# Performance work log

Hardware: AMD Instinct MI355X
Metric: run time of the kernel (lower is better)

## Reference

```python
import jax, jax.numpy as jnp
import numpy as np

B, SEQ, NNODES = 4, 12, 1024
SEG_LEN, SEG_NUM = 3, 4
HID, FF, DK, NH, NLAYERS = 64, 2048, 32, 8, 2


def setup_inputs() -> dict:
    key = jax.random.key(0)
    ks = iter(jax.random.split(key, 64))
    def nrm(shape, scale=0.05):
        return jax.random.normal(next(ks), shape, dtype=jnp.float32) * scale
    ones = lambda s: jnp.ones(s, jnp.float32)
    zeros = lambda s: jnp.zeros(s, jnp.float32)
    S, L = 2, NLAYERS
    return {
        'traffic': nrm((B, SEQ, NNODES), 1.0),
        'user': nrm((B, SEQ, NNODES), 1.0),
        'patch_w': nrm((S, HID, SEG_LEN)), 'patch_b': nrm((S, HID)),
        'mha_w': nrm((S, L, 3 * HID, HID)), 'mha_b': nrm((S, L, 3 * HID)),
        'out_w': nrm((S, L, HID, HID)), 'out_b': nrm((S, L, HID)),
        'ff1_w': nrm((S, L, FF, HID)), 'ff1_b': nrm((S, L, FF)),
        'ff2_w': nrm((S, L, HID, FF)), 'ff2_b': nrm((S, L, HID)),
        'ln1_g': ones((S, L, HID)), 'ln1_b': zeros((S, L, HID)),
        'ln2_g': ones((S, L, HID)), 'ln2_b': zeros((S, L, HID)),
        'ga_wq': nrm((S, L, DK, HID)), 'ga_wk': nrm((S, L, DK, HID)), 'ga_wv': nrm((S, L, HID, HID)),
        'ga_ff1_w': nrm((S, L, FF, HID)), 'ga_ff1_b': nrm((S, L, FF)),
        'ga_ff2_w': nrm((S, L, HID, FF)), 'ga_ff2_b': nrm((S, L, HID)),
        'ga_ln1_g': ones((S, L, HID)), 'ga_ln1_b': zeros((S, L, HID)),
        'ga_ln2_g': ones((S, L, HID)), 'ga_ln2_b': zeros((S, L, HID)),
        'ca_wq': nrm((DK, 2 * HID)), 'ca_wk': nrm((DK, 2 * HID)), 'ca_wv': nrm((HID, 2 * HID)),
    }


def _ln(x, g, b, eps=1e-5):
    m = x.mean(-1, keepdims=True)
    v = jnp.mean((x - m) ** 2, -1, keepdims=True)
    return (x - m) / jnp.sqrt(v + eps) * g + b


def _pe(s, d):
    pos = jnp.arange(s, dtype=jnp.float32)[:, None]
    div = jnp.exp(jnp.arange(0, d, 2, dtype=jnp.float32) * (-np.log(10000.0) / d))
    pe = jnp.zeros((s, d), jnp.float32)
    pe = pe.at[:, 0::2].set(jnp.sin(pos * div))
    pe = pe.at[:, 1::2].set(jnp.cos(pos * div))
    return pe


def _mha(x, w, b, wo, bo):
    # standard nn.MultiheadAttention self-attn, batch_first; x: [B,S,H]
    qkv = x @ w.T + b
    q, k, v = jnp.split(qkv, 3, axis=-1)
    def heads(t):
        b_, s_, h_ = t.shape
        return t.reshape(b_, s_, NH, h_ // NH).transpose(0, 2, 1, 3)
    q, k, v = heads(q), heads(k), heads(v)
    scale = 1.0 / jnp.sqrt(jnp.float32(HID // NH))
    att = jax.nn.softmax(jnp.einsum('bhqd,bhkd->bhqk', q, k) * scale, axis=-1)
    o = jnp.einsum('bhqk,bhkd->bhqd', att, v).transpose(0, 2, 1, 3).reshape(x.shape)
    return o @ wo.T + bo


def _enc_layer(x, p):
    # TransformerEncoderLayer_cross, post-norm, dropout=0 (eval)
    x = _ln(x + _mha(x, p['mw'], p['mb'], p['ow'], p['ob']), p['g1'], p['b1'])
    f = jax.nn.relu(x @ p['f1w'].T + p['f1b']) @ p['f2w'].T + p['f2b']
    return _ln(x + f, p['g2'], p['b2'])


def _graph_att(x, p):
    # GraphAttention.forward (bias=None, mask=None, dropout=0)
    q = x @ p['wq'].T
    k = x @ p['wk'].T
    v = x @ p['wv'].T
    dist = jax.nn.softmax(jnp.einsum('bnd,bmd->bnm', q, k) / jnp.sqrt(jnp.float32(DK)), axis=-1)
    att = jnp.einsum('bnm,bmd->bnd', dist, v)
    att = _ln(att, p['g1'], p['b1']) + x
    f = jax.nn.relu(att @ p['f1w'].T + p['f1b']) @ p['f2w'].T + p['f2b']
    return _ln(att + f, p['g2'], p['b2'])


def reference(traffic, user, patch_w, patch_b, mha_w, mha_b, out_w, out_b,
              ff1_w, ff1_b, ff2_w, ff2_b, ln1_g, ln1_b, ln2_g, ln2_b,
              ga_wq, ga_wk, ga_wv, ga_ff1_w, ga_ff1_b, ga_ff2_w, ga_ff2_b,
              ga_ln1_g, ga_ln1_b, ga_ln2_g, ga_ln2_b, ca_wq, ca_wk, ca_wv):
    pe = _pe(SEG_NUM, HID)

    def encode(x, s):
        b, _, d = x.shape
        # DSW_embedding: b (seg_num seg_len) d -> b d seg_num seg_len, then Linear
        seg = x.reshape(b, SEG_NUM, SEG_LEN, d).transpose(0, 3, 1, 2)
        z = seg @ patch_w[s].T + patch_b[s]          # [b, d, seg_num, HID]
        z = z + pe                                    # positional encoding over patches
        for i in range(NLAYERS):
            # temporal attention over the patch axis
            zt = z.reshape(b * d, SEG_NUM, HID)
            zt = _enc_layer(zt, dict(mw=mha_w[s, i], mb=mha_b[s, i], ow=out_w[s, i], ob=out_b[s, i],
                                     f1w=ff1_w[s, i], f1b=ff1_b[s, i], f2w=ff2_w[s, i], f2b=ff2_b[s, i],
                                     g1=ln1_g[s, i], b1=ln1_b[s, i], g2=ln2_g[s, i], b2=ln2_b[s, i]))
            z = zt.reshape(b, d, SEG_NUM, HID)
            # spatial graph attention over the node axis
            zs = z.transpose(0, 2, 1, 3).reshape(b * SEG_NUM, d, HID)
            zs = _graph_att(zs, dict(wq=ga_wq[s, i], wk=ga_wk[s, i], wv=ga_wv[s, i],
                                     f1w=ga_ff1_w[s, i], f1b=ga_ff1_b[s, i], f2w=ga_ff2_w[s, i], f2b=ga_ff2_b[s, i],
                                     g1=ga_ln1_g[s, i], b1=ga_ln1_b[s, i], g2=ga_ln2_g[s, i], b2=ga_ln2_b[s, i]))
            z = zs.reshape(b, SEG_NUM, d, HID).transpose(0, 2, 1, 3)
        return z.mean(axis=2)                         # pool patches -> [b, d, HID]

    enc = jnp.concatenate([encode(traffic, 0), encode(user, 1)], axis=-1)  # [b, d, 2*HID]
    # encoder_attn: SelfAttention(2*HID -> dim_k=32, dim_v=HID)
    q = enc @ ca_wq.T
    k = enc @ ca_wk.T
    v = enc @ ca_wv.T
    dist = jax.nn.softmax(jnp.einsum('bnd,bmd->bnm', q, k) / jnp.sqrt(jnp.float32(DK)), axis=-1)
    return jnp.einsum('bnm,bmd->bnd', dist, v)        # [b, n_nodes, HID]
```

## Files before the change

kernel.cpp:

```cpp
#include <hip/hip_runtime.h>
#include <hip/hip_bf16.h>
#include <math.h>

#define BB 4
#define SEQL 12
#define NN 1024
#define SEGL 3
#define SEGN 4
#define HID 64
#define FFD 2048
#define DKK 32
#define NHH 8
#define HDD 8
#define ZS 1048576

using bf16 = __hip_bfloat16;
__device__ __forceinline__ float b2f(bf16 v) { return __bfloat162float(v); }

typedef __attribute__((ext_vector_type(8))) short s8v;
typedef __attribute__((ext_vector_type(4))) float f4v;
typedef __attribute__((ext_vector_type(4))) unsigned short u4v;

__device__ __forceinline__ unsigned short f2b(float f) {
  bf16 h = __float2bfloat16(f);
  unsigned short u; __builtin_memcpy(&u, &h, 2); return u;
}
__device__ __forceinline__ float us2f(unsigned short u) {
  unsigned int e = ((unsigned int)u) << 16;
  float f; __builtin_memcpy(&f, &e, 4); return f;
}

template <int F>
__device__ __forceinline__ float ldw(const void* p, long i) {
  if (F) return ((const float*)p)[i];
  return b2f(((const bf16*)p)[i]);
}
template <int F>
__device__ __forceinline__ s8v ldfrag(const void* p, long elemOff) {
  if (F) {
    const float* fp = (const float*)p + elemOff;
    f4v u = *(const f4v*)fp, v = *(const f4v*)(fp + 4);
    s8v t;
    t[0]=f2b(u[0]); t[1]=f2b(u[1]); t[2]=f2b(u[2]); t[3]=f2b(u[3]);
    t[4]=f2b(v[0]); t[5]=f2b(v[1]); t[6]=f2b(v[2]); t[7]=f2b(v[3]);
    return t;
  }
  return *(const s8v*)((const unsigned short*)p + elemOff);
}
template <int F>
__device__ __forceinline__ f4v ldb4(const void* p, long i) {
  if (F) return *(const f4v*)((const float*)p + i);
  u4v u = *(const u4v*)((const unsigned short*)p + i);
  f4v r; r[0]=us2f(u[0]); r[1]=us2f(u[1]); r[2]=us2f(u[2]); r[3]=us2f(u[3]);
  return r;
}

__global__ void k_zero(unsigned short* __restrict__ o, int n) {
  int i = blockIdx.x * 256 + threadIdx.x;
  if (i < n) o[i] = 0;
}

__global__ void k_detect(const void* __restrict__ x0, int* __restrict__ flag) {
  int t = threadIdx.x;
  int bad = 0;
  const bf16* p = (const bf16*)x0;
  for (int i = t; i < 512; i += 256) {
    float a = fabsf(b2f(p[i]));
    if (!(a < 1e4f) || (a != 0.f && a < 1e-4f)) bad = 1;
  }
  __shared__ int tot;
  if (t == 0) tot = 0;
  __syncthreads();
  unsigned long long m = __ballot(bad);
  if ((t & 63) == 0) atomicAdd(&tot, __popcll(m));
  __syncthreads();
  if (t == 0) *flag = (tot > 64) ? 1 : 0;
}

template <int F>
__device__ __forceinline__ void wconv_body(const void* __restrict__ w1,
    const void* __restrict__ w2, const void* __restrict__ w3,
    const void* __restrict__ w4, unsigned short* __restrict__ out) {
  int i = blockIdx.x * 256 + threadIdx.x;
  long e8 = (long)i * 8;
  int slot = (int)(e8 >> 17);
  int si = slot >> 2, which = slot & 3;
  long r = e8 & 131071;
  const void* src = (which == 0) ? w1 : (which == 1) ? w2 : (which == 2) ? w3 : w4;
  *(s8v*)(out + e8) = ldfrag<F>(src, (long)si*FFD*HID + r);
}
__global__ __launch_bounds__(256) void k_wconv(const void* w1, const void* w2,
    const void* w3, const void* w4, unsigned short* out,
    const int* __restrict__ flag) {
  if (*flag) wconv_body<1>(w1, w2, w3, w4, out);
  else       wconv_body<0>(w1, w2, w3, w4, out);
}

template <int F>
__device__ __forceinline__ void patch_body(const void* __restrict__ xt,
    const void* __restrict__ xu,
    const void* __restrict__ pw, const void* __restrict__ pb,
    float* __restrict__ z) {
  int bid = blockIdx.x;
  int s = bid >> 12, rem = bid & 4095;
  int b = rem >> 10, n = rem & 1023;
  const void* x = s ? xu : xt;
  long opw = (long)s*HID*SEGL, opb = (long)s*HID;
  int g = threadIdx.x >> 6, h = threadIdx.x & 63;
  float acc = ldw<F>(pb, opb + h);
#pragma unroll
  for (int l = 0; l < SEGL; ++l)
    acc += ldw<F>(x, (long)(b*SEQL + g*SEGL + l)*NN + n) * ldw<F>(pw, opw + h*SEGL + l);
  int i2 = h >> 1;
  float dv = expf((float)(2*i2) * (-logf(10000.f) / (float)HID));
  float ang = (float)g * dv;
  acc += (h & 1) ? cosf(ang) : sinf(ang);
  z[(long)s*ZS + ((long)(b*NN + n)*SEGN + g)*HID + h] = acc;
}
__global__ __launch_bounds__(256) void k_patch(const void* __restrict__ xt,
    const void* __restrict__ xu,
    const void* __restrict__ pw, const void* __restrict__ pb,
    float* __restrict__ z, const int* __restrict__ flag) {
  if (*flag) patch_body<1>(xt, xu, pw, pb, z);
  else       patch_body<0>(xt, xu, pw, pb, z);
}

#define TT 64
template <int F>
__device__ __forceinline__ void tattn_body(float* __restrict__ zb,
    const void* __restrict__ W, const void* __restrict__ bq,
    const void* __restrict__ WO, const void* __restrict__ bo,
    const void* __restrict__ g1, const void* __restrict__ b1,
    int li, char* lds) {
  int s = blockIdx.x >> 8, blk = blockIdx.x & 255;
  long si = s*2 + li;
  float* z = zb + (long)s*ZS;
  long oW = si*3*HID*HID, obq = si*3*HID, oWO = si*HID*HID, obo = si*HID;
  long og1 = si*HID, ob1 = si*HID;
  unsigned short (*qkvs)[200] = (unsigned short(*)[200])lds;
  unsigned short (*ao)[72]    = (unsigned short(*)[72])(lds + 25600);
  float (*yb)[68]             = (float(*)[68])(lds + 34816);
  int tid = threadIdx.x;
  int w = tid >> 6, lane = tid & 63;
  int col = lane & 15, quad = lane >> 4;
  long r0 = (long)blk * TT;

  s8v bx[4][2];
#pragma unroll
  for (int mt = 0; mt < 4; ++mt) {
    const float* xr = z + (r0 + mt*16 + col) * HID;
#pragma unroll
    for (int ks = 0; ks < 2; ++ks) {
      const float* p = xr + ks*32 + quad*8;
      f4v u = *(const f4v*)p, v = *(const f4v*)(p + 4);
      s8v t;
      t[0]=f2b(u[0]); t[1]=f2b(u[1]); t[2]=f2b(u[2]); t[3]=f2b(u[3]);
      t[4]=f2b(v[0]); t[5]=f2b(v[1]); t[6]=f2b(v[2]); t[7]=f2b(v[3]);
      bx[mt][ks] = t;
    }
  }
#pragma unroll
  for (int nt = 0; nt < 3; ++nt) {
    int cbase = (w*3 + nt) * 16;
    s8v aw[2];
#pragma unroll
    for (int ks = 0; ks < 2; ++ks)
      aw[ks] = ldfrag<F>(W, oW + (long)(cbase + col)*HID + ks*32 + quad*8);
    f4v bv = ldb4<F>(bq, obq + cbase + quad*4);
#pragma unroll
    for (int mt = 0; mt < 4; ++mt) {
      f4v sv = (f4v){0.f,0.f,0.f,0.f};
#pragma unroll
      for (int ks = 0; ks < 2; ++ks)
        sv = __builtin_amdgcn_mfma_f32_16x16x32_bf16(aw[ks], bx[mt][ks], sv, 0, 0, 0);
      unsigned short pk[4];
#pragma unroll
      for (int r = 0; r < 4; ++r) pk[r] = f2b(sv[r] + bv[r]);
      *(unsigned long long*)&qkvs[mt*16 + col][cbase + quad*4] =
        (unsigned long long)pk[0] | ((unsigned long long)pk[1] << 16) |
        ((unsigned long long)pk[2] << 32) | ((unsigned long long)pk[3] << 48);
    }
  }
  __syncthreads();
  if (tid < 128) {
    int gi = tid >> 3, hd = tid & 7;
    int tl = gi * 4;
    float qv[4][8], kv[4][8], vv[4][8];
#pragma unroll
    for (int t4 = 0; t4 < 4; ++t4) {
      s8v qq = *(const s8v*)&qkvs[tl + t4][hd*8];
      s8v kk = *(const s8v*)&qkvs[tl + t4][64 + hd*8];
      s8v vq = *(const s8v*)&qkvs[tl + t4][128 + hd*8];
#pragma unroll
      for (int e = 0; e < 8; ++e) {
        qv[t4][e] = us2f((unsigned short)qq[e]);
        kv[t4][e] = us2f((unsigned short)kk[e]);
        vv[t4][e] = us2f((unsigned short)vq[e]);
      }
    }
    const float sc8 = 0.3535533905932738f;
#pragma unroll
    for (int qt = 0; qt < 4; ++qt) {
      float s[4]; float mx = -1e30f;
#pragma unroll
      for (int kt = 0; kt < 4; ++kt) {
        float d = 0;
#pragma unroll
        for (int e = 0; e < 8; ++e) d += qv[qt][e]*kv[kt][e];
        s[kt] = d*sc8; mx = fmaxf(mx, s[kt]);
      }
      float se = 0;
#pragma unroll
      for (int kt = 0; kt < 4; ++kt) { s[kt] = expf(s[kt]-mx); se += s[kt]; }
      float inv = 1.f/se;
      s8v outp;
#pragma unroll
      for (int e = 0; e < 8; ++e) {
        float o = 0;
#pragma unroll
        for (int kt = 0; kt < 4; ++kt) o += s[kt]*vv[kt][e];
        outp[e] = (short)f2b(o*inv);
      }
      *(s8v*)&ao[tl + qt][hd*8] = outp;
    }
  }
  __syncthreads();
  s8v awo[2];
#pragma unroll
  for (int ks = 0; ks < 2; ++ks)
    awo[ks] = ldfrag<F>(WO, oWO + (long)(w*16 + col)*HID + ks*32 + quad*8);
  f4v bov = ldb4<F>(bo, obo + w*16 + quad*4);
#pragma unroll
  for (int mt = 0; mt < 4; ++mt) {
    f4v ov = (f4v){0.f,0.f,0.f,0.f};
#pragma unroll
    for (int ks = 0; ks < 2; ++ks) {
      s8v bao = *(const s8v*)&ao[mt*16 + col][ks*32 + quad*8];
      ov = __builtin_amdgcn_mfma_f32_16x16x32_bf16(awo[ks], bao, ov, 0, 0, 0);
    }
    f4v yv;
#pragma unroll
    for (int r = 0; r < 4; ++r) yv[r] = ov[r] + bov[r];
    *(f4v*)&yb[mt*16 + col][w*16 + quad*4] = yv;
  }
  __syncthreads();
  float gg = ldw<F>(g1, og1 + lane), bb2 = ldw<F>(b1, ob1 + lane);
#pragma unroll
  for (int rr = 0; rr < 16; ++rr) {
    int row = w*16 + rr;
    long tok = r0 + row;
    float val = yb[row][lane] + z[tok*HID + lane];
    float s = val;
#pragma unroll
    for (int off = 32; off; off >>= 1) s += __shfl_xor(s, off);
    float m = s*(1.f/HID);
    float d = val - m, sq = d*d;
#pragma unroll
    for (int off = 32; off; off >>= 1) sq += __shfl_xor(sq, off);
    float rv = rsqrtf(sq*(1.f/HID) + 1e-5f);
    z[tok*HID + lane] = d*rv*gg + bb2;
  }
}
__global__ __launch_bounds__(256) void k_tattn(float* __restrict__ z,
    const void* W, const void* bqkv, const void* WO, const void* bo,
    const void* g1, const void* b1, int li, const int* __restrict__ flag) {
  __shared__ __attribute__((aligned(16))) char lds[52224];
  if (*flag) tattn_body<1>(z, W, bqkv, WO, bo, g1, b1, li, lds);
  else       tattn_body<0>(z, W, bqkv, WO, bo, g1, b1, li, lds);
}

#define FRW 64
#define HCS 74

__device__ __forceinline__ void ff_ld(const unsigned short* __restrict__ wc1,
    const unsigned short* __restrict__ wc2, int hb, int srow, int le,
    s8v* r1, s8v* r2) {
  r1[0] = *(const s8v*)(wc1 + (long)(hb + srow)*HID + le*8);
  r1[1] = *(const s8v*)(wc1 + (long)(hb + srow + 8)*HID + le*8);
  r2[0] = *(const s8v*)(wc2 + (long)srow*FFD + hb + le*8);
  r2[1] = *(const s8v*)(wc2 + (long)(srow + 8)*FFD + hb + le*8);
}
__device__ __forceinline__ void ff_wr(char* ldsbuf, int pb, int srow, int swb,
    const s8v* r1, const s8v* r2) {
  char* w1b = ldsbuf + pb*8192;
  char* w2b = ldsbuf + 16384 + pb*8192;
  *(s8v*)(w1b + srow*128 + swb) = r1[0];
  *(s8v*)(w1b + (srow + 8)*128 + swb) = r1[1];
  *(s8v*)(w2b + srow*128 + swb) = r2[0];
  *(s8v*)(w2b + (srow + 8)*128 + swb) = r2[1];
}

template <int F>
__device__ __forceinline__ void ffmfma_body(float* __restrict__ xb,
    const unsigned short* __restrict__ wcw, int li, int wsel,
    const void* __restrict__ B1, const void* __restrict__ B2,
    const void* __restrict__ G, const void* __restrict__ Bt,
    char* ldsbuf) {
  int s = blockIdx.x >> 8, blk = blockIdx.x & 255;
  long si = s*2 + li;
  float* x = xb + (long)s*ZS;
  const unsigned short* wc1 = wcw + (si*4 + wsel)*131072;
  const unsigned short* wc2 = wcw + (si*4 + wsel + 1)*131072;
  long ob1 = si*FFD, ob2 = si*HID, og = si*HID, obt = si*HID;
  int tid = threadIdx.x;
  int w = tid >> 6, lane = tid & 63;
  int col = lane & 15, quad = lane >> 4;
  long r0 = (long)blk * FRW;
  unsigned short* hcw = (unsigned short*)(ldsbuf + 32768 + w*2368);
  float* red = (float*)(ldsbuf + 42240 + w*4352);

  long tokc = r0 + w*16 + col;
  s8v bx[2];
  {
    const float* xr = x + tokc * HID;
#pragma unroll
    for (int ks = 0; ks < 2; ++ks) {
      const float* p = xr + ks*32 + quad*8;
      f4v u = *(const f4v*)p, v = *(const f4v*)(p + 4);
      s8v t;
      t[0]=f2b(u[0]); t[1]=f2b(u[1]); t[2]=f2b(u[2]); t[3]=f2b(u[3]);
      t[4]=f2b(v[0]); t[5]=f2b(v[1]); t[6]=f2b(v[2]); t[7]=f2b(v[3]);
      bx[ks] = t;
    }
  }

  int lr = lane >> 3;
  int le = lane & 7;
  int srow = w*16 + lr;
  int swb = ((le ^ lr) << 4);

  f4v acc[4];
#pragma unroll
  for (int m = 0; m < 4; ++m) acc[m] = (f4v){0.f,0.f,0.f,0.f};

  s8v cw1[2], cw2[2], nw1[2], nw2[2];
  ff_ld(wc1, wc2, 0, srow, le, cw1, cw2);
  ff_wr(ldsbuf, 0, srow, swb, cw1, cw2);
  __syncthreads();

  const int sw = (col & 7) << 4;
  for (int c = 0; c < 32; ++c) {
    int pb = c & 1;
    if (c < 31) ff_ld(wc1, wc2, (c+1)*64, srow, le, nw1, nw2);
    const char* w1b = ldsbuf + pb*8192;
    const char* w2b = ldsbuf + 16384 + pb*8192;
    const int hb = c*64;
#pragma unroll
    for (int t = 0; t < 4; ++t) {
      int row = t*16 + col;
      s8v a10 = *(const s8v*)(w1b + row*128 + ((quad*16) ^ sw));
      s8v a11 = *(const s8v*)(w1b + row*128 + ((64 + quad*16) ^ sw));
      f4v bv = ldb4<F>(B1, ob1 + hb + t*16 + quad*4);
      f4v sv = __builtin_amdgcn_mfma_f32_16x16x32_bf16(a10, bx[0],
                 (f4v){0.f,0.f,0.f,0.f}, 0, 0, 0);
      sv = __builtin_amdgcn_mfma_f32_16x16x32_bf16(a11, bx[1], sv, 0, 0, 0);
      unsigned short pk[4];
#pragma unroll
      for (int r = 0; r < 4; ++r) pk[r] = f2b(fmaxf(sv[r] + bv[r], 0.f));
      *(unsigned long long*)&hcw[col*HCS + t*16 + quad*4] =
        (unsigned long long)pk[0] | ((unsigned long long)pk[1] << 16) |
        ((unsigned long long)pk[2] << 32) | ((unsigned long long)pk[3] << 48);
    }
#pragma unroll
    for (int ks2 = 0; ks2 < 2; ++ks2) {
      s8v bh = *(const s8v*)&hcw[col*HCS + ks2*32 + quad*8];
#pragma unroll
      for (int m = 0; m < 4; ++m) {
        int r2 = m*16 + col;
        s8v a2 = *(const s8v*)(w2b + r2*128 + ((ks2*64 + quad*16) ^ sw));
        acc[m] = __builtin_amdgcn_mfma_f32_16x16x32_bf16(a2, bh, acc[m], 0, 0, 0);
      }
    }
    if (c < 31) ff_wr(ldsbuf, pb ^ 1, srow, swb, nw1, nw2);
    __syncthreads();
  }

#pragma unroll
  for (int m = 0; m < 4; ++m)
    *(f4v*)&red[col*68 + m*16 + quad*4] = acc[m];
  float gg = ldw<F>(G, og + lane), bbt = ldw<F>(Bt, obt + lane);
  float b2v = ldw<F>(B2, ob2 + lane);
#pragma unroll
  for (int rr = 0; rr < 16; ++rr) {
    long grow = r0 + w*16 + rr;
    float val = red[rr*68 + lane] + b2v + x[grow*HID + lane];
    float sm = val;
#pragma unroll
    for (int off = 32; off; off >>= 1) sm += __shfl_xor(sm, off);
    float m = sm * (1.f/HID);
    float d = val - m;
    float sq = d*d;
#pragma unroll
    for (int off = 32; off; off >>= 1) sq += __shfl_xor(sq, off);
    float rv = rsqrtf(sq*(1.f/HID) + 1e-5f);
    x[grow*HID + lane] = d*rv*gg + bbt;
  }
}
__global__ __launch_bounds__(256) void k_ffmfma(float* __restrict__ x,
    const unsigned short* __restrict__ wcw, int li, int wsel,
    const void* B1, const void* B2, const void* G, const void* Bt,
    const int* __restrict__ flag) {
  __shared__ __attribute__((aligned(16))) char ldsbuf[59648];
  if (*flag) ffmfma_body<1>(x, wcw, li, wsel, B1, B2, G, Bt, ldsbuf);
  else       ffmfma_body<0>(x, wcw, li, wsel, B1, B2, G, Bt, ldsbuf);
}

template <int F>
__device__ __forceinline__ void gqkv_body(const float* __restrict__ zb,
    const void* __restrict__ wq, const void* __restrict__ wk,
    const void* __restrict__ wv, int li,
    unsigned short* __restrict__ q, unsigned short* __restrict__ k,
    unsigned short* __restrict__ vt) {
  int tid = threadIdx.x;
  int w = tid >> 6, lane = tid & 63;
  int col = lane & 15, quad = lane >> 4;
  int sg = blockIdx.x >> 4;
  int s = sg >> 4, bg = sg & 15;
  int n0 = (blockIdx.x & 15) * 64;
  int b = bg >> 2, g = bg & 3;
  long si = s*2 + li;
  const float* z = zb + (long)s*ZS;
  long oq = si*DKK*HID, ok = si*DKK*HID, ov = si*HID*HID;
  long gbase = (long)sg * NN;

  s8v bx[4][2];
#pragma unroll
  for (int rt = 0; rt < 4; ++rt) {
    const float* xr = z + ((long)(b*NN + n0 + rt*16 + col)*SEGN + g)*HID;
#pragma unroll
    for (int ks = 0; ks < 2; ++ks) {
      const float* p = xr + ks*32 + quad*8;
      f4v u = *(const f4v*)p, vv = *(const f4v*)(p + 4);
      s8v t;
      t[0]=f2b(u[0]); t[1]=f2b(u[1]); t[2]=f2b(u[2]); t[3]=f2b(u[3]);
      t[4]=f2b(vv[0]); t[5]=f2b(vv[1]); t[6]=f2b(vv[2]); t[7]=f2b(vv[3]);
      bx[rt][ks] = t;
    }
  }

#pragma unroll
  for (int tt = 0; tt < 2; ++tt) {
    int ct = w*2 + tt;
    const void* wp; long wo; int co; int kind;
    if (ct < 2)      { wp = wq; wo = oq; co = ct*16;      kind = 0; }
    else if (ct < 4) { wp = wk; wo = ok; co = (ct-2)*16;  kind = 1; }
    else             { wp = wv; wo = ov; co = (ct-4)*16;  kind = 2; }
    s8v aw[2];
#pragma unroll
    for (int ks = 0; ks < 2; ++ks)
      aw[ks] = ldfrag<F>(wp, wo + (long)(co + col)*HID + ks*32 + quad*8);
#pragma unroll
    for (int rt = 0; rt < 4; ++rt) {
      f4v sv = (f4v){0.f,0.f,0.f,0.f};
#pragma unroll
      for (int ks = 0; ks < 2; ++ks)
        sv = __builtin_amdgcn_mfma_f32_16x16x32_bf16(aw[ks], bx[rt][ks], sv, 0, 0, 0);
      int key = n0 + rt*16 + col;
      if (kind == 2) {
        long vbase = (long)sg*HID*NN;
#pragma unroll
        for (int r = 0; r < 4; ++r)
          vt[vbase + (long)(co + quad*4 + r)*NN + key] = f2b(sv[r]);
      } else {
        long row = gbase + key;
        unsigned short pk[4];
#pragma unroll
        for (int r = 0; r < 4; ++r) pk[r] = f2b(sv[r]);
        unsigned short* dst = kind ? k : q;
        *(unsigned long long*)&dst[row*DKK + co + quad*4] =
          (unsigned long long)pk[0] | ((unsigned long long)pk[1] << 16) |
          ((unsigned long long)pk[2] << 32) | ((unsigned long long)pk[3] << 48);
      }
    }
  }
}
__global__ __launch_bounds__(256) void k_gqkv(const float* __restrict__ z,
    const void* wq, const void* wk, const void* wv, int li,
    unsigned short* q, unsigned short* k, unsigned short* vt,
    const int* __restrict__ flag) {
  if (*flag) gqkv_body<1>(z, wq, wk, wv, li, q, k, vt);
  else       gqkv_body<0>(z, wq, wk, wv, li, q, k, vt);
}

__global__ __launch_bounds__(512) void k_gattn(float* __restrict__ zb,
    const unsigned short* __restrict__ qb, const unsigned short* __restrict__ kb,
    const unsigned short* __restrict__ vtb,
    const void* __restrict__ g1, const void* __restrict__ b1, int li,
    const int* __restrict__ flag) {
  int f = *flag;
  __shared__ unsigned short pl[2][8][16][74];
  __shared__ float accb[8][16][66];
  __shared__ float lb[8][16];
  int tid = threadIdx.x;
  int w = tid >> 6, lane = tid & 63;
  int col = lane & 15, quad = lane >> 4;
  int qt = w >> 1, kh = w & 1;
  int sg = blockIdx.x >> 4;
  int s = sg >> 4, bg = sg & 15;
  int n0 = (blockIdx.x & 15) * 64;
  long si = s*2 + li;
  float* z = zb + (long)s*ZS;
  long og1 = si*HID, ob1 = si*HID;
  long gbase = (long)sg * NN;
  const unsigned short* vrow = vtb + (long)sg*HID*NN;

  s8v aq = *(const s8v*)(qb + (gbase + n0 + qt*16 + col)*DKK + quad*8);

  f4v acc[4];
#pragma unroll
  for (int t = 0; t < 4; ++t) acc[t] = (f4v){0.f,0.f,0.f,0.f};
  float psum[4] = {0.f,0.f,0.f,0.f};
  const float rs = 0.17677669529663687f;
  const int cbeg = kh * 512;

#pragma unroll 2
  for (int it = 0; it < 8; ++it) {
    int c0 = cbeg + it*64;
    int pb = it & 1;
    f4v s4[4];
#pragma unroll
    for (int nt = 0; nt < 4; ++nt) {
      s8v bk = *(const s8v*)(kb + (gbase + c0 + nt*16 + col)*DKK + quad*8);
      s4[nt] = __builtin_amdgcn_mfma_f32_16x16x32_bf16(aq, bk,
                (f4v){0.f,0.f,0.f,0.f}, 0, 0, 0);
    }
#pragma unroll
    for (int r = 0; r < 4; ++r) {
      float p0 = expf(s4[0][r]*rs), p1 = expf(s4[1][r]*rs);
      float p2 = expf(s4[2][r]*rs), p3 = expf(s4[3][r]*rs);
      psum[r] += (p0 + p1) + (p2 + p3);
      int row = quad*4 + r;
      pl[pb][w][row][col]      = f2b(p0);
      pl[pb][w][row][16 + col] = f2b(p1);
      pl[pb][w][row][32 + col] = f2b(p2);
      pl[pb][w][row][48 + col] = f2b(p3);
    }
#pragma unroll
    for (int ks = 0; ks < 2; ++ks) {
      s8v ap = *(const s8v*)&pl[pb][w][col][ks*32 + quad*8];
#pragma unroll
      for (int nt = 0; nt < 4; ++nt) {
        s8v bv = *(const s8v*)(vrow + (long)(nt*16 + col)*NN + c0 + ks*32 + quad*8);
        acc[nt] = __builtin_amdgcn_mfma_f32_16x16x32_bf16(ap, bv, acc[nt], 0, 0, 0);
      }
    }
  }

#pragma unroll
  for (int r = 0; r < 4; ++r) {
    float v = psum[r];
#pragma unroll
    for (int off = 1; off < 16; off <<= 1) v += __shfl_xor(v, off);
    psum[r] = v;
  }
#pragma unroll
  for (int t = 0; t < 4; ++t)
#pragma unroll
    for (int r = 0; r < 4; ++r)
      accb[w][quad*4 + r][t*16 + col] = acc[t][r];
  if (col == 0) {
#pragma unroll
    for (int r = 0; r < 4; ++r) lb[w][quad*4 + r] = psum[r];
  }
  __syncthreads();

  int b = bg >> 2, g = bg & 3;
  float gg = f ? ((const float*)g1)[og1 + lane] : b2f(((const bf16*)g1)[og1 + lane]);
  float bb = f ? ((const float*)b1)[ob1 + lane] : b2f(((const bf16*)b1)[ob1 + lane]);
#pragma unroll
  for (int rr = 0; rr < 8; ++rr) {
    int rl = w*8 + rr;
    int qtt = rl >> 4, lr = rl & 15;
    float a = accb[2*qtt][lr][lane] + accb[2*qtt + 1][lr][lane];
    float l = lb[2*qtt][lr] + lb[2*qtt + 1][lr];
    float val = a / l;
    float s = val;
#pragma unroll
    for (int off = 32; off; off >>= 1) s += __shfl_xor(s, off);
    float m = s*(1.f/HID);
    float d = val - m, sq = d*d;
#pragma unroll
    for (int off = 32; off; off >>= 1) sq += __shfl_xor(sq, off);
    float r = rsqrtf(sq*(1.f/HID) + 1e-5f);
    float* zp = z + ((long)(b*NN + n0 + rl)*SEGN + g)*HID;
    zp[lane] = d*r*gg + bb + zp[lane];
  }
}

__global__ __launch_bounds__(64) void k_pool(const float* __restrict__ z,
    float* __restrict__ enc) {
  int bid = blockIdx.x;
  int s = bid >> 12, rem = bid & 4095;
  int b = rem >> 10, n = rem & 1023, h = threadIdx.x;
  const float* zp = z + (long)s*ZS + (long)(b*NN + n)*SEGN*HID;
  float a = 0;
#pragma unroll
  for (int g = 0; g < SEGN; ++g) a += zp[g*HID + h];
  enc[(long)(b*NN + n)*(2*HID) + s*HID + h] = a*0.25f;
}

template <int F>
__device__ __forceinline__ void fqkv_body(const float* __restrict__ enc,
    const void* __restrict__ wq, const void* __restrict__ wk,
    const void* __restrict__ wv,
    unsigned short* __restrict__ q, unsigned short* __restrict__ k,
    unsigned short* __restrict__ vt, float* xs) {
  long r = blockIdx.x;
  int t = threadIdx.x;
  xs[t] = enc[r*128 + t];
  __syncthreads();
  if (t < 32) {
    long wr = (long)t*128; float a = 0;
    for (int e = 0; e < 128; ++e) a += xs[e]*ldw<F>(wq, wr + e);
    q[r*DKK + t] = f2b(a);
  } else if (t < 64) {
    long wr = (long)(t-32)*128; float a = 0;
    for (int e = 0; e < 128; ++e) a += xs[e]*ldw<F>(wk, wr + e);
    k[r*DKK + (t-32)] = f2b(a);
  } else {
    long wr = (long)(t-64)*128; float a = 0;
    for (int e = 0; e < 128; ++e) a += xs[e]*ldw<F>(wv, wr + e);
    vt[((r >> 10)*HID + (t-64))*NN + (r & 1023)] = f2b(a);
  }
}
__global__ __launch_bounds__(128) void k_fqkv(const float* __restrict__ enc,
    const void* wq, const void* wk, const void* wv,
    unsigned short* q, unsigned short* k, unsigned short* vt,
    const int* __restrict__ flag) {
  __shared__ float xs[2*HID];
  if (*flag) fqkv_body<1>(enc, wq, wk, wv, q, k, vt, xs);
  else       fqkv_body<0>(enc, wq, wk, wv, q, k, vt, xs);
}

__global__ __launch_bounds__(512) void k_fattn(
    const unsigned short* __restrict__ qb, const unsigned short* __restrict__ kb,
    const unsigned short* __restrict__ vtb, void* __restrict__ outp,
    const int* __restrict__ flag) {
  __shared__ unsigned short pl[2][8][16][74];
  __shared__ float accb[8][16][66];
  __shared__ float lb[8][16];
  int tid = threadIdx.x;
  int w = tid >> 6, lane = tid & 63;
  int col = lane & 15, quad = lane >> 4;
  int qt = w >> 1, kh = w & 1;
  int b = blockIdx.x >> 4;
  int n0 = (blockIdx.x & 15) * 64;
  long gbase = (long)b * NN;
  const unsigned short* vrow = vtb + (long)b*HID*NN;

  s8v aq = *(const s8v*)(qb + (gbase + n0 + qt*16 + col)*DKK + quad*8);

  f4v acc[4];
#pragma unroll
  for (int t = 0; t < 4; ++t) acc[t] = (f4v){0.f,0.f,0.f,0.f};
  float psum[4] = {0.f,0.f,0.f,0.f};
  const float rs = 0.17677669529663687f;
  const int cbeg = kh * 512;

#pragma unroll 2
  for (int it = 0; it < 8; ++it) {
    int c0 = cbeg + it*64;
    int pb = it & 1;
    f4v s4[4];
#pragma unroll
    for (int nt = 0; nt < 4; ++nt) {
      s8v bk = *(const s8v*)(kb + (gbase + c0 + nt*16 + col)*DKK + quad*8);
      s4[nt] = __builtin_amdgcn_mfma_f32_16x16x32_bf16(aq, bk,
                (f4v){0.f,0.f,0.f,0.f}, 0, 0, 0);
    }
#pragma unroll
    for (int r = 0; r < 4; ++r) {
      float p0 = expf(s4[0][r]*rs), p1 = expf(s4[1][r]*rs);
      float p2 = expf(s4[2][r]*rs), p3 = expf(s4[3][r]*rs);
      psum[r] += (p0 + p1) + (p2 + p3);
      int row = quad*4 + r;
      pl[pb][w][row][col]      = f2b(p0);
      pl[pb][w][row][16 + col] = f2b(p1);
      pl[pb][w][row][32 + col] = f2b(p2);
      pl[pb][w][row][48 + col] = f2b(p3);
    }
#pragma unroll
    for (int ks = 0; ks < 2; ++ks) {
      s8v ap = *(const s8v*)&pl[pb][w][col][ks*32 + quad*8];
#pragma unroll
      for (int nt = 0; nt < 4; ++nt) {
        s8v bv = *(const s8v*)(vrow + (long)(nt*16 + col)*NN + c0 + ks*32 + quad*8);
        acc[nt] = __builtin_amdgcn_mfma_f32_16x16x32_bf16(ap, bv, acc[nt], 0, 0, 0);
      }
    }
  }

#pragma unroll
  for (int r = 0; r < 4; ++r) {
    float v = psum[r];
#pragma unroll
    for (int off = 1; off < 16; off <<= 1) v += __shfl_xor(v, off);
    psum[r] = v;
  }
#pragma unroll
  for (int t = 0; t < 4; ++t)
#pragma unroll
    for (int r = 0; r < 4; ++r)
      accb[w][quad*4 + r][t*16 + col] = acc[t][r];
  if (col == 0) {
#pragma unroll
    for (int r = 0; r < 4; ++r) lb[w][quad*4 + r] = psum[r];
  }
  __syncthreads();

  int f = *flag;
#pragma unroll
  for (int rr = 0; rr < 8; ++rr) {
    int rl = w*8 + rr;
    int qtt = rl >> 4, lr = rl & 15;
    float a = accb[2*qtt][lr][lane] + accb[2*qtt + 1][lr][lane];
    float l = lb[2*qtt][lr] + lb[2*qtt + 1][lr];
    float val = a / l;
    long idx = (gbase + n0 + rl)*HID + lane;
    if (f) ((float*)outp)[idx] = val;
    else   ((bf16*)outp)[idx] = __float2bfloat16(val);
  }
}

extern "C" void kernel_launch(void* const* d_in, const int* in_sizes, int n_in,
                              void* d_out, int out_size, void* d_ws, size_t ws_size,
                              hipStream_t stream) {
  static const int EXP[30] = {
    49152, 49152, 384, 128, 49152, 768, 16384, 256,
    524288, 8192, 524288, 256, 256, 256, 256, 256,
    8192, 8192, 16384, 524288, 8192, 524288, 256, 256,
    256, 256, 256, 4096, 4096, 8192
  };
  const size_t NEED = (size_t)(2*ZS + 524288 + 524288 + 524288 + 1048576 + 1048576) * 4 + 64;
  bool ok = (n_in == 30) && (ws_size >= NEED) && (out_size == BB*NN*HID);
  if (ok) for (int i = 0; i < 30; ++i) ok = ok && (in_sizes[i] == EXP[i]);
  if (!ok) {
    k_zero<<<(BB*NN*HID + 255)/256, 256, 0, stream>>>((unsigned short*)d_out, BB*NN*HID);
    return;
  }

  float* z   = (float*)d_ws;
  float* enc = z   + 2*ZS;
  float* qb  = enc + 524288;
  float* kb  = qb  + 524288;
  float* vb  = kb  + 524288;
  float* wcf = vb  + 1048576;
  int*  flag = (int*)(wcf + 1048576);
  unsigned short* wcw = (unsigned short*)wcf;

  k_detect<<<1, 256, 0, stream>>>(d_in[0], flag);

  const void *i_traffic=d_in[0], *i_user=d_in[1], *i_pw=d_in[2], *i_pb=d_in[3],
    *i_mw=d_in[4], *i_mb=d_in[5], *i_ow=d_in[6], *i_ob=d_in[7], *i_f1w=d_in[8],
    *i_f1b=d_in[9], *i_f2w=d_in[10], *i_f2b=d_in[11], *i_l1g=d_in[12],
    *i_l1b=d_in[13], *i_l2g=d_in[14], *i_l2b=d_in[15], *i_gwq=d_in[16],
    *i_gwk=d_in[17], *i_gwv=d_in[18], *i_gf1w=d_in[19], *i_gf1b=d_in[20],
    *i_gf2w=d_in[21], *i_gf2b=d_in[22], *i_gl1g=d_in[23], *i_gl1b=d_in[24],
    *i_gl2g=d_in[25], *i_gl2b=d_in[26], *i_cwq=d_in[27], *i_cwk=d_in[28],
    *i_cwv=d_in[29];

  k_wconv<<<1024, 256, 0, stream>>>(i_f1w, i_f2w, i_gf1w, i_gf2w, wcw, flag);
  k_patch<<<2*BB*NN, 256, 0, stream>>>(i_traffic, i_user, i_pw, i_pb, z, flag);

  const int FFG = 2*BB*NN*SEGN/FRW;

  for (int i = 0; i < 2; ++i) {
    k_tattn<<<512, 256, 0, stream>>>(z, i_mw, i_mb, i_ow, i_ob,
        i_l1g, i_l1b, i, flag);
    k_ffmfma<<<FFG, 256, 0, stream>>>(z, wcw, i, 0,
        i_f1b, i_f2b, i_l2g, i_l2b, flag);
    k_gqkv<<<512, 256, 0, stream>>>(z, i_gwq, i_gwk, i_gwv, i,
        (unsigned short*)qb, (unsigned short*)kb, (unsigned short*)vb, flag);
    k_gattn<<<512, 512, 0, stream>>>(z,
        (const unsigned short*)qb, (const unsigned short*)kb,
        (const unsigned short*)vb, i_gl1g, i_gl1b, i, flag);
    k_ffmfma<<<FFG, 256, 0, stream>>>(z, wcw, i, 2,
        i_gf1b, i_gf2b, i_gl2g, i_gl2b, flag);
  }
  k_pool<<<2*BB*NN, 64, 0, stream>>>(z, enc);
  k_fqkv<<<BB*NN, 128, 0, stream>>>(enc, i_cwq, i_cwk, i_cwv,
      (unsigned short*)qb, (unsigned short*)kb, (unsigned short*)vb, flag);
  k_fattn<<<BB*16, 512, 0, stream>>>((const unsigned short*)qb,
      (const unsigned short*)kb, (unsigned short*)vb, d_out, flag);
}
```

Before: 610.1 us.

## Fuse temporal attention with feed-forward and fold patch pooling into final FFN

Merges the temporal self-attention kernel and the following feed-forward kernel into one kernel. The post-LayerNorm activations stay in shared memory instead of being written to and re-read from global memory, which also removes one launch per layer. Separately, the last graph FFN epilogue now accumulates the segment mean and writes the pooled encoding directly, so the standalone pooling kernel is dropped. The fused kernel uses more shared memory (about 77KB per block), which may lower occupancy.

Measured after the change: 601.4 us. Within noise of the previous version (-1.4%).

```diff
diff --git a/kernel.cpp b/kernel.cpp
--- a/kernel.cpp
+++ b/kernel.cpp
@@ -126,149 +126,6 @@
 }
 
 #define TT 64
-template <int F>
-__device__ __forceinline__ void tattn_body(float* __restrict__ zb,
-    const void* __restrict__ W, const void* __restrict__ bq,
-    const void* __restrict__ WO, const void* __restrict__ bo,
-    const void* __restrict__ g1, const void* __restrict__ b1,
-    int li, char* lds) {
-  int s = blockIdx.x >> 8, blk = blockIdx.x & 255;
-  long si = s*2 + li;
-  float* z = zb + (long)s*ZS;
-  long oW = si*3*HID*HID, obq = si*3*HID, oWO = si*HID*HID, obo = si*HID;
-  long og1 = si*HID, ob1 = si*HID;
-  unsigned short (*qkvs)[200] = (unsigned short(*)[200])lds;
-  unsigned short (*ao)[72]    = (unsigned short(*)[72])(lds + 25600);
-  float (*yb)[68]             = (float(*)[68])(lds + 34816);
-  int tid = threadIdx.x;
-  int w = tid >> 6, lane = tid & 63;
-  int col = lane & 15, quad = lane >> 4;
-  long r0 = (long)blk * TT;
-
-  s8v bx[4][2];
-#pragma unroll
-  for (int mt = 0; mt < 4; ++mt) {
-    const float* xr = z + (r0 + mt*16 + col) * HID;
-#pragma unroll
-    for (int ks = 0; ks < 2; ++ks) {
-      const float* p = xr + ks*32 + quad*8;
-      f4v u = *(const f4v*)p, v = *(const f4v*)(p + 4);
-      s8v t;
-      t[0]=f2b(u[0]); t[1]=f2b(u[1]); t[2]=f2b(u[2]); t[3]=f2b(u[3]);
-      t[4]=f2b(v[0]); t[5]=f2b(v[1]); t[6]=f2b(v[2]); t[7]=f2b(v[3]);
-      bx[mt][ks] = t;
-    }
-  }
-#pragma unroll
-  for (int nt = 0; nt < 3; ++nt) {
-    int cbase = (w*3 + nt) * 16;
-    s8v aw[2];
-#pragma unroll
-    for (int ks = 0; ks < 2; ++ks)
-      aw[ks] = ldfrag<F>(W, oW + (long)(cbase + col)*HID + ks*32 + quad*8);
-    f4v bv = ldb4<F>(bq, obq + cbase + quad*4);
-#pragma unroll
-    for (int mt = 0; mt < 4; ++mt) {
-      f4v sv = (f4v){0.f,0.f,0.f,0.f};
-#pragma unroll
-      for (int ks = 0; ks < 2; ++ks)
-        sv = __builtin_amdgcn_mfma_f32_16x16x32_bf16(aw[ks], bx[mt][ks], sv, 0, 0, 0);
-      unsigned short pk[4];
-#pragma unroll
-      for (int r = 0; r < 4; ++r) pk[r] = f2b(sv[r] + bv[r]);
-      *(unsigned long long*)&qkvs[mt*16 + col][cbase + quad*4] =
-        (unsigned long long)pk[0] | ((unsigned long long)pk[1] << 16) |
-        ((unsigned long long)pk[2] << 32) | ((unsigned long long)pk[3] << 48);
-    }
-  }
-  __syncthreads();
-  if (tid < 128) {
-    int gi = tid >> 3, hd = tid & 7;
-    int tl = gi * 4;
-    float qv[4][8], kv[4][8], vv[4][8];
-#pragma unroll
-    for (int t4 = 0; t4 < 4; ++t4) {
-      s8v qq = *(const s8v*)&qkvs[tl + t4][hd*8];
-      s8v kk = *(const s8v*)&qkvs[tl + t4][64 + hd*8];
-      s8v vq = *(const s8v*)&qkvs[tl + t4][128 + hd*8];
-#pragma unroll
-      for (int e = 0; e < 8; ++e) {
-        qv[t4][e] = us2f((unsigned short)qq[e]);
-        kv[t4][e] = us2f((unsigned short)kk[e]);
-        vv[t4][e] = us2f((unsigned short)vq[e]);
-      }
-    }
-    const float sc8 = 0.3535533905932738f;
-#pragma unroll
-    for (int qt = 0; qt < 4; ++qt) {
-      float s[4]; float mx = -1e30f;
-#pragma unroll
-      for (int kt = 0; kt < 4; ++kt) {
-        float d = 0;
-#pragma unroll
-        for (int e = 0; e < 8; ++e) d += qv[qt][e]*kv[kt][e];
-        s[kt] = d*sc8; mx = fmaxf(mx, s[kt]);
-      }
-      float se = 0;
-#pragma unroll
-      for (int kt = 0; kt < 4; ++kt) { s[kt] = expf(s[kt]-mx); se += s[kt]; }
-      float inv = 1.f/se;
-      s8v outp;
-#pragma unroll
-      for (int e = 0; e < 8; ++e) {
-        float o = 0;
-#pragma unroll
-        for (int kt = 0; kt < 4; ++kt) o += s[kt]*vv[kt][e];
-        outp[e] = (short)f2b(o*inv);
-      }
-      *(s8v*)&ao[tl + qt][hd*8] = outp;
-    }
-  }
-  __syncthreads();
-  s8v awo[2];
-#pragma unroll
-  for (int ks = 0; ks < 2; ++ks)
-    awo[ks] = ldfrag<F>(WO, oWO + (long)(w*16 + col)*HID + ks*32 + quad*8);
-  f4v bov = ldb4<F>(bo, obo + w*16 + quad*4);
-#pragma unroll
-  for (int mt = 0; mt < 4; ++mt) {
-    f4v ov = (f4v){0.f,0.f,0.f,0.f};
-#pragma unroll
-    for (int ks = 0; ks < 2; ++ks) {
-      s8v bao = *(const s8v*)&ao[mt*16 + col][ks*32 + quad*8];
-      ov = __builtin_amdgcn_mfma_f32_16x16x32_bf16(awo[ks], bao, ov, 0, 0, 0);
-    }
-    f4v yv;
-#pragma unroll
-    for (int r = 0; r < 4; ++r) yv[r] = ov[r] + bov[r];
-    *(f4v*)&yb[mt*16 + col][w*16 + quad*4] = yv;
-  }
-  __syncthreads();
-  float gg = ldw<F>(g1, og1 + lane), bb2 = ldw<F>(b1, ob1 + lane);
-#pragma unroll
-  for (int rr = 0; rr < 16; ++rr) {
-    int row = w*16 + rr;
-    long tok = r0 + row;
-    float val = yb[row][lane] + z[tok*HID + lane];
-    float s = val;
-#pragma unroll
-    for (int off = 32; off; off >>= 1) s += __shfl_xor(s, off);
-    float m = s*(1.f/HID);
-    float d = val - m, sq = d*d;
-#pragma unroll
-    for (int off = 32; off; off >>= 1) sq += __shfl_xor(sq, off);
-    float rv = rsqrtf(sq*(1.f/HID) + 1e-5f);
-    z[tok*HID + lane] = d*rv*gg + bb2;
-  }
-}
-__global__ __launch_bounds__(256) void k_tattn(float* __restrict__ z,
-    const void* W, const void* bqkv, const void* WO, const void* bo,
-    const void* g1, const void* b1, int li, const int* __restrict__ flag) {
-  __shared__ __attribute__((aligned(16))) char lds[52224];
-  if (*flag) tattn_body<1>(z, W, bqkv, WO, bo, g1, b1, li, lds);
-  else       tattn_body<0>(z, W, bqkv, WO, bo, g1, b1, li, lds);
-}
-
 #define FRW 64
 #define HCS 74
 
@@ -291,10 +148,253 @@
 }
 
 template <int F>
+__device__ __forceinline__ void tff_body(float* __restrict__ zb,
+    const void* __restrict__ W, const void* __restrict__ bq,
+    const void* __restrict__ WO, const void* __restrict__ bo,
+    const void* __restrict__ g1, const void* __restrict__ b1,
+    const unsigned short* __restrict__ wcw, int li,
+    const void* __restrict__ B1, const void* __restrict__ B2,
+    const void* __restrict__ G, const void* __restrict__ Bt,
+    char* lds) {
+  int s = blockIdx.x >> 8, blk = blockIdx.x & 255;
+  long si = s*2 + li;
+  float* z = zb + (long)s*ZS;
+  long oW = si*3*HID*HID, obq = si*3*HID, oWO = si*HID*HID, obo = si*HID;
+  long og1 = si*HID, ob1 = si*HID;
+  const unsigned short* wc1 = wcw + (si*4 + 0)*131072;
+  const unsigned short* wc2 = wcw + (si*4 + 1)*131072;
+  long fob1 = si*FFD, fob2 = si*HID, fog = si*HID, fobt = si*HID;
+  unsigned short (*qkvs)[200] = (unsigned short(*)[200])lds;
+  unsigned short (*ao)[72]    = (unsigned short(*)[72])(lds + 25600);
+  float (*yb)[68]             = (float(*)[68])(lds + 34816);
+  int tid = threadIdx.x;
+  int w = tid >> 6, lane = tid & 63;
+  int col = lane & 15, quad = lane >> 4;
+  long r0 = (long)blk * TT;
+  float* stashW = (float*)(lds + 59648 + w*4352);
+
+  int lr = lane >> 3, le = lane & 7;
+  int srow = w*16 + lr;
+  int swb = ((le ^ lr) << 4);
+  s8v cw1[2], cw2[2];
+  ff_ld(wc1, wc2, 0, srow, le, cw1, cw2);
+
+  s8v bx[4][2];
+#pragma unroll
+  for (int mt = 0; mt < 4; ++mt) {
+    const float* xr = z + (r0 + mt*16 + col) * HID;
+#pragma unroll
+    for (int ks = 0; ks < 2; ++ks) {
+      const float* p = xr + ks*32 + quad*8;
+      f4v u = *(const f4v*)p, v = *(const f4v*)(p + 4);
+      s8v t;
+      t[0]=f2b(u[0]); t[1]=f2b(u[1]); t[2]=f2b(u[2]); t[3]=f2b(u[3]);
+      t[4]=f2b(v[0]); t[5]=f2b(v[1]); t[6]=f2b(v[2]); t[7]=f2b(v[3]);
+      bx[mt][ks] = t;
+    }
+  }
+#pragma unroll
+  for (int nt = 0; nt < 3; ++nt) {
+    int cbase = (w*3 + nt) * 16;
+    s8v aw[2];
+#pragma unroll
+    for (int ks = 0; ks < 2; ++ks)
+      aw[ks] = ldfrag<F>(W, oW + (long)(cbase + col)*HID + ks*32 + quad*8);
+    f4v bv = ldb4<F>(bq, obq + cbase + quad*4);
+#pragma unroll
+    for (int mt = 0; mt < 4; ++mt) {
+      f4v sv = (f4v){0.f,0.f,0.f,0.f};
+#pragma unroll
+      for (int ks = 0; ks < 2; ++ks)
+        sv = __builtin_amdgcn_mfma_f32_16x16x32_bf16(aw[ks], bx[mt][ks], sv, 0, 0, 0);
+      unsigned short pk[4];
+#pragma unroll
+      for (int r = 0; r < 4; ++r) pk[r] = f2b(sv[r] + bv[r]);
+      *(unsigned long long*)&qkvs[mt*16 + col][cbase + quad*4] =
+        (unsigned long long)pk[0] | ((unsigned long long)pk[1] << 16) |
+        ((unsigned long long)pk[2] << 32) | ((unsigned long long)pk[3] << 48);
+    }
+  }
+  __syncthreads();
+  if (tid < 128) {
+    int gi = tid >> 3, hd = tid & 7;
+    int tl = gi * 4;
+    float qv[4][8], kv[4][8], vv[4][8];
+#pragma unroll
+    for (int t4 = 0; t4 < 4; ++t4) {
+      s8v qq = *(const s8v*)&qkvs[tl + t4][hd*8];
+      s8v kk = *(const s8v*)&qkvs[tl + t4][64 + hd*8];
+      s8v vq = *(const s8v*)&qkvs[tl + t4][128 + hd*8];
+#pragma unroll
+      for (int e = 0; e < 8; ++e) {
+        qv[t4][e] = us2f((unsigned short)qq[e]);
+        kv[t4][e] = us2f((unsigned short)kk[e]);
+        vv[t4][e] = us2f((unsigned short)vq[e]);
+      }
+    }
+    const float sc8 = 0.3535533905932738f;
+#pragma unroll
+    for (int qt = 0; qt < 4; ++qt) {
+      float sc[4]; float mx = -1e30f;
+#pragma unroll
+      for (int kt = 0; kt < 4; ++kt) {
+        float d = 0;
+#pragma unroll
+        for (int e = 0; e < 8; ++e) d += qv[qt][e]*kv[kt][e];
+        sc[kt] = d*sc8; mx = fmaxf(mx, sc[kt]);
+      }
+      float se = 0;
+#pragma unroll
+      for (int kt = 0; kt < 4; ++kt) { sc[kt] = expf(sc[kt]-mx); se += sc[kt]; }
+      float inv = 1.f/se;
+      s8v outp;
+#pragma unroll
+      for (int e = 0; e < 8; ++e) {
+        float o = 0;
+#pragma unroll
+        for (int kt = 0; kt < 4; ++kt) o += sc[kt]*vv[kt][e];
+        outp[e] = (short)f2b(o*inv);
+      }
+      *(s8v*)&ao[tl + qt][hd*8] = outp;
+    }
+  }
+  __syncthreads();
+  s8v awo[2];
+#pragma unroll
+  for (int ks = 0; ks < 2; ++ks)
+    awo[ks] = ldfrag<F>(WO, oWO + (long)(w*16 + col)*HID + ks*32 + quad*8);
+  f4v bov = ldb4<F>(bo, obo + w*16 + quad*4);
+#pragma unroll
+  for (int mt = 0; mt < 4; ++mt) {
+    f4v ov = (f4v){0.f,0.f,0.f,0.f};
+#pragma unroll
+    for (int ks = 0; ks < 2; ++ks) {
+      s8v bao = *(const s8v*)&ao[mt*16 + col][ks*32 + quad*8];
+      ov = __builtin_amdgcn_mfma_f32_16x16x32_bf16(awo[ks], bao, ov, 0, 0, 0);
+    }
+    f4v yv;
+#pragma unroll
+    for (int r = 0; r < 4; ++r) yv[r] = ov[r] + bov[r];
+    *(f4v*)&yb[mt*16 + col][w*16 + quad*4] = yv;
+  }
+  __syncthreads();
+  {
+    float gg = ldw<F>(g1, og1 + lane), bb2 = ldw<F>(b1, ob1 + lane);
+#pragma unroll
+    for (int rr = 0; rr < 16; ++rr) {
+      int row = w*16 + rr;
+      long tok = r0 + row;
+      float val = yb[row][lane] + z[tok*HID + lane];
+      float sm = val;
+#pragma unroll
+      for (int off = 32; off; off >>= 1) sm += __shfl_xor(sm, off);
+      float m = sm*(1.f/HID);
+      float d = val - m, sq = d*d;
+#pragma unroll
+      for (int off = 32; off; off >>= 1) sq += __shfl_xor(sq, off);
+      float rv = rsqrtf(sq*(1.f/HID) + 1e-5f);
+      stashW[rr*68 + lane] = d*rv*gg + bb2;
+    }
+  }
+  __syncthreads();
+
+  unsigned short* hcw = (unsigned short*)(lds + 32768 + w*2368);
+  float* red = (float*)(lds + 42240 + w*4352);
+
+  s8v bx2[2];
+#pragma unroll
+  for (int ks = 0; ks < 2; ++ks) {
+    const float* p = &stashW[col*68 + ks*32 + quad*8];
+    f4v u = *(const f4v*)p, v = *(const f4v*)(p + 4);
+    s8v t;
+    t[0]=f2b(u[0]); t[1]=f2b(u[1]); t[2]=f2b(u[2]); t[3]=f2b(u[3]);
+    t[4]=f2b(v[0]); t[5]=f2b(v[1]); t[6]=f2b(v[2]); t[7]=f2b(v[3]);
+    bx2[ks] = t;
+  }
+
+  f4v acc[4];
+#pragma unroll
+  for (int m = 0; m < 4; ++m) acc[m] = (f4v){0.f,0.f,0.f,0.f};
+
+  ff_wr(lds, 0, srow, swb, cw1, cw2);
+  __syncthreads();
+
+  const int sw = (col & 7) << 4;
+  s8v nw1[2], nw2[2];
+  for (int c = 0; c < 32; ++c) {
+    int pb = c & 1;
+    if (c < 31) ff_ld(wc1, wc2, (c+1)*64, srow, le, nw1, nw2);
+    const char* w1b = lds + pb*8192;
+    const char* w2b = lds + 16384 + pb*8192;
+    const int hb = c*64;
+#pragma unroll
+    for (int t = 0; t < 4; ++t) {
+      int row = t*16 + col;
+      s8v a10 = *(const s8v*)(w1b + row*128 + ((quad*16) ^ sw));
+      s8v a11 = *(const s8v*)(w1b + row*128 + ((64 + quad*16) ^ sw));
+      f4v bv = ldb4<F>(B1, fob1 + hb + t*16 + quad*4);
+      f4v sv = __builtin_amdgcn_mfma_f32_16x16x32_bf16(a10, bx2[0],
+                 (f4v){0.f,0.f,0.f,0.f}, 0, 0, 0);
+      sv = __builtin_amdgcn_mfma_f32_16x16x32_bf16(a11, bx2[1], sv, 0, 0, 0);
+      unsigned short pk[4];
+#pragma unroll
+      for (int r = 0; r < 4; ++r) pk[r] = f2b(fmaxf(sv[r] + bv[r], 0.f));
+      *(unsigned long long*)&hcw[col*HCS + t*16 + quad*4] =
+        (unsigned long long)pk[0] | ((unsigned long long)pk[1] << 16) |
+        ((unsigned long long)pk[2] << 32) | ((unsigned long long)pk[3] << 48);
+    }
+#pragma unroll
+    for (int ks2 = 0; ks2 < 2; ++ks2) {
+      s8v bh = *(const s8v*)&hcw[col*HCS + ks2*32 + quad*8];
+#pragma unroll
+      for (int m = 0; m < 4; ++m) {
+        int r2 = m*16 + col;
+        s8v a2 = *(const s8v*)(w2b + r2*128 + ((ks2*64 + quad*16) ^ sw));
+        acc[m] = __builtin_amdgcn_mfma_f32_16x16x32_bf16(a2, bh, acc[m], 0, 0, 0);
+      }
+    }
+    if (c < 31) ff_wr(lds, pb ^ 1, srow, swb, nw1, nw2);
+    __syncthreads();
+  }
+
+#pragma unroll
+  for (int m = 0; m < 4; ++m)
+    *(f4v*)&red[col*68 + m*16 + quad*4] = acc[m];
+  float fgg = ldw<F>(G, fog + lane), fbbt = ldw<F>(Bt, fobt + lane);
+  float b2v = ldw<F>(B2, fob2 + lane);
+#pragma unroll
+  for (int rr = 0; rr < 16; ++rr) {
+    long grow = r0 + w*16 + rr;
+    float val = red[rr*68 + lane] + b2v + stashW[rr*68 + lane];
+    float sm = val;
+#pragma unroll
+    for (int off = 32; off; off >>= 1) sm += __shfl_xor(sm, off);
+    float m = sm * (1.f/HID);
+    float d = val - m;
+    float sq = d*d;
+#pragma unroll
+    for (int off = 32; off; off >>= 1) sq += __shfl_xor(sq, off);
+    float rv = rsqrtf(sq*(1.f/HID) + 1e-5f);
+    z[grow*HID + lane] = d*rv*fgg + fbbt;
+  }
+}
+__global__ __launch_bounds__(256) void k_tff(float* __restrict__ z,
+    const void* W, const void* bqkv, const void* WO, const void* bo,
+    const void* g1, const void* b1,
+    const unsigned short* __restrict__ wcw, int li,
+    const void* B1, const void* B2, const void* G, const void* Bt,
+    const int* __restrict__ flag) {
+  __shared__ __attribute__((aligned(16))) char lds[77056];
+  if (*flag) tff_body<1>(z, W, bqkv, WO, bo, g1, b1, wcw, li, B1, B2, G, Bt, lds);
+  else       tff_body<0>(z, W, bqkv, WO, bo, g1, b1, wcw, li, B1, B2, G, Bt, lds);
+}
+
+template <int F>
 __device__ __forceinline__ void ffmfma_body(float* __restrict__ xb,
     const unsigned short* __restrict__ wcw, int li, int wsel,
     const void* __restrict__ B1, const void* __restrict__ B2,
     const void* __restrict__ G, const void* __restrict__ Bt,
+    float* __restrict__ enc, int dop,
     char* ldsbuf) {
   int s = blockIdx.x >> 8, blk = blockIdx.x & 255;
   long si = s*2 + li;
@@ -380,6 +480,7 @@
     *(f4v*)&red[col*68 + m*16 + quad*4] = acc[m];
   float gg = ldw<F>(G, og + lane), bbt = ldw<F>(Bt, obt + lane);
   float b2v = ldw<F>(B2, ob2 + lane);
+  float pacc[4] = {0.f,0.f,0.f,0.f};
 #pragma unroll
   for (int rr = 0; rr < 16; ++rr) {
     long grow = r0 + w*16 + rr;
@@ -393,16 +494,25 @@
 #pragma unroll
     for (int off = 32; off; off >>= 1) sq += __shfl_xor(sq, off);
     float rv = rsqrtf(sq*(1.f/HID) + 1e-5f);
-    x[grow*HID + lane] = d*rv*gg + bbt;
+    float fin = d*rv*gg + bbt;
+    x[grow*HID + lane] = fin;
+    pacc[rr >> 2] += fin;
+  }
+  if (dop) {
+#pragma unroll
+    for (int j = 0; j < 4; ++j) {
+      long tok = r0 + w*16 + j*4;
+      enc[(tok >> 2)*(2*HID) + s*HID + lane] = pacc[j]*0.25f;
+    }
   }
 }
 __global__ __launch_bounds__(256) void k_ffmfma(float* __restrict__ x,
     const unsigned short* __restrict__ wcw, int li, int wsel,
     const void* B1, const void* B2, const void* G, const void* Bt,
-    const int* __restrict__ flag) {
+    float* enc, int dop, const int* __restrict__ flag) {
   __shared__ __attribute__((aligned(16))) char ldsbuf[59648];
-  if (*flag) ffmfma_body<1>(x, wcw, li, wsel, B1, B2, G, Bt, ldsbuf);
-  else       ffmfma_body<0>(x, wcw, li, wsel, B1, B2, G, Bt, ldsbuf);
+  if (*flag) ffmfma_body<1>(x, wcw, li, wsel, B1, B2, G, Bt, enc, dop, ldsbuf);
+  else       ffmfma_body<0>(x, wcw, li, wsel, B1, B2, G, Bt, enc, dop, ldsbuf);
 }
 
 template <int F>
@@ -574,10 +684,10 @@
     float a = accb[2*qtt][lr][lane] + accb[2*qtt + 1][lr][lane];
     float l = lb[2*qtt][lr] + lb[2*qtt + 1][lr];
     float val = a / l;
-    float s = val;
-#pragma unroll
-    for (int off = 32; off; off >>= 1) s += __shfl_xor(s, off);
-    float m = s*(1.f/HID);
+    float s2 = val;
+#pragma unroll
+    for (int off = 32; off; off >>= 1) s2 += __shfl_xor(s2, off);
+    float m = s2*(1.f/HID);
     float d = val - m, sq = d*d;
 #pragma unroll
     for (int off = 32; off; off >>= 1) sq += __shfl_xor(sq, off);
@@ -585,18 +695,6 @@
     float* zp = z + ((long)(b*NN + n0 + rl)*SEGN + g)*HID;
     zp[lane] = d*r*gg + bb + zp[lane];
   }
-}
-
-__global__ __launch_bounds__(64) void k_pool(const float* __restrict__ z,
-    float* __restrict__ enc) {
-  int bid = blockIdx.x;
-  int s = bid >> 12, rem = bid & 4095;
-  int b = rem >> 10, n = rem & 1023, h = threadIdx.x;
-  const float* zp = z + (long)s*ZS + (long)(b*NN + n)*SEGN*HID;
-  float a = 0;
-#pragma unroll
-  for (int g = 0; g < SEGN; ++g) a += zp[g*HID + h];
-  enc[(long)(b*NN + n)*(2*HID) + s*HID + h] = a*0.25f;
 }
 
 template <int F>
@@ -762,22 +860,17 @@
   k_wconv<<<1024, 256, 0, stream>>>(i_f1w, i_f2w, i_gf1w, i_gf2w, wcw, flag);
   k_patch<<<2*BB*NN, 256, 0, stream>>>(i_traffic, i_user, i_pw, i_pb, z, flag);
 
-  const int FFG = 2*BB*NN*SEGN/FRW;
-
   for (int i = 0; i < 2; ++i) {
-    k_tattn<<<512, 256, 0, stream>>>(z, i_mw, i_mb, i_ow, i_ob,
-        i_l1g, i_l1b, i, flag);
-    k_ffmfma<<<FFG, 256, 0, stream>>>(z, wcw, i, 0,
-        i_f1b, i_f2b, i_l2g, i_l2b, flag);
+    k_tff<<<512, 256, 0, stream>>>(z, i_mw, i_mb, i_ow, i_ob,
+        i_l1g, i_l1b, wcw, i, i_f1b, i_f2b, i_l2g, i_l2b, flag);
     k_gqkv<<<512, 256, 0, stream>>>(z, i_gwq, i_gwk, i_gwv, i,
         (unsigned short*)qb, (unsigned short*)kb, (unsigned short*)vb, flag);
     k_gattn<<<512, 512, 0, stream>>>(z,
         (const unsigned short*)qb, (const unsigned short*)kb,
         (const unsigned short*)vb, i_gl1g, i_gl1b, i, flag);
-    k_ffmfma<<<FFG, 256, 0, stream>>>(z, wcw, i, 2,
-        i_gf1b, i_gf2b, i_gl2g, i_gl2b, flag);
-  }
-  k_pool<<<2*BB*NN, 64, 0, stream>>>(z, enc);
+    k_ffmfma<<<512, 256, 0, stream>>>(z, wcw, i, 2,
+        i_gf1b, i_gf2b, i_gl2g, i_gl2b, enc, (i == 1) ? 1 : 0, flag);
+  }
   k_fqkv<<<BB*NN, 128, 0, stream>>>(enc, i_cwq, i_cwk, i_cwv,
       (unsigned short*)qb, (unsigned short*)kb, (unsigned short*)vb, flag);
   k_fattn<<<BB*16, 512, 0, stream>>>((const unsigned short*)qb,
```
